# Performance work log

Measured on AMD Instinct MI355X. Metric: run time of the kernel, lower is better.

The kernel has to match this reference:

```python
import jax, jax.numpy as jnp
import numpy as np

N_EMBD = 1024
N_HEAD = 16
HEAD_DIM = N_EMBD // N_HEAD
SEQ = 2048
BATCH = 2
WINDOW = 256
SCALE = 1.0 / np.sqrt(HEAD_DIM)
MASK_VALUE = -10000.0


def setup_inputs() -> dict:
    key = jax.random.key(0)
    ks = jax.random.split(key, 5)
    s = 0.02
    return {
        "hidden_states": jax.random.normal(ks[0], (BATCH, SEQ, N_EMBD), dtype=jnp.float32),
        "w_attn": jax.random.normal(ks[1], (N_EMBD, 3 * N_EMBD), dtype=jnp.float32) * s,
        "b_attn": jnp.zeros((3 * N_EMBD,), dtype=jnp.float32),
        "w_proj": jax.random.normal(ks[2], (N_EMBD, N_EMBD), dtype=jnp.float32) * s,
        "b_proj": jnp.zeros((N_EMBD,), dtype=jnp.float32),
    }


def _mask(seq_len):
    # causal AND sliding window: j <= i and j > i - WINDOW
    i = jnp.arange(seq_len)[:, None]
    j = jnp.arange(seq_len)[None, :]
    return (j <= i) & (j > i - WINDOW)  # [T, T] bool


def reference(hidden_states, w_attn, b_attn, w_proj, b_proj):
    B, T, _ = hidden_states.shape
    qkv = hidden_states @ w_attn + b_attn  # [B, T, 3E]
    q, k, v = jnp.split(qkv, 3, axis=-1)
    # [B, H, T, D]
    q = q.reshape(B, T, N_HEAD, HEAD_DIM).transpose(0, 2, 1, 3)
    k = k.reshape(B, T, N_HEAD, HEAD_DIM).transpose(0, 2, 1, 3)
    v = v.reshape(B, T, N_HEAD, HEAD_DIM).transpose(0, 2, 1, 3)

    scores = jnp.einsum("bhqd,bhkd->bhqk", q, k) * SCALE  # [B, H, T, T]
    mask = _mask(T)[None, None]  # [1, 1, T, T]
    scores = jnp.where(mask, scores, MASK_VALUE)
    scores = jnp.clip(scores, -10000.0, 10000.0)
    attn = jax.nn.softmax(scores, axis=-1)
    out = jnp.einsum("bhqk,bhkd->bhqd", attn, v)  # [B, H, T, D]
    out = out.transpose(0, 2, 1, 3).reshape(B, T, N_EMBD)
    return out @ w_proj + b_proj
```

## Files before the change

### kernel.cpp

```cpp
#include <hip/hip_runtime.h>


typedef __bf16 bf16_t;
typedef bf16_t bf16x8 __attribute__((ext_vector_type(8)));
typedef bf16_t bf16x4 __attribute__((ext_vector_type(4)));
typedef float  floatx4 __attribute__((ext_vector_type(4)));

#define SEQ_T   2048
#define NHEAD   16
#define HDIM    64
#define EMB     1024
#define WIN     256
#define SCALE_F 0.125f

__device__ __forceinline__ int detect_bf16(const uint4* __restrict__ det)
{
    const int lane = threadIdx.x & 63;
    const uint4 v = det[lane];
    int c = 0;
    #pragma unroll
    for (int e = 0; e < 4; ++e) {
        const unsigned int ex = ((&v.x)[e] >> 7) & 0xffu;
        c += (ex >= 100u && ex <= 150u) ? 1 : 0;
    }
    #pragma unroll
    for (int m = 32; m >= 1; m >>= 1) c += __shfl_xor(c, m, 64);
    return (c * 2 > 256) ? 1 : 0;
}

__global__ __launch_bounds__(256) void prologue(
    const void* __restrict__ hidden, bf16_t* __restrict__ Hc,
    const void* __restrict__ ba, bf16_t* __restrict__ bba,
    const void* __restrict__ bp, bf16_t* __restrict__ bbp,
    const void* __restrict__ wA, bf16_t* __restrict__ WtA,
    const void* __restrict__ wP, bf16_t* __restrict__ WtP)
{
    __shared__ __align__(16) bf16_t tile[64][68];
    const int f = detect_bf16((const uint4*)hidden);
    const int blk = blockIdx.x;

    if (blk < 4100) {
        if (f) return;
        const float* src;
        bf16_t* dst;
        int base;
        if (blk < 4096)      { src = (const float*)hidden; dst = Hc;  base = blk * 1024; }
        else if (blk < 4099) { src = (const float*)ba;     dst = bba; base = (blk - 4096) * 1024; }
        else                 { src = (const float*)bp;     dst = bbp; base = 0; }
        const int i4 = base + threadIdx.x * 4;
        const float4 x = *(const float4*)(src + i4);
        bf16x4 v;
        v[0] = (bf16_t)x.x; v[1] = (bf16_t)x.y;
        v[2] = (bf16_t)x.z; v[3] = (bf16_t)x.w;
        *(bf16x4*)(dst + i4) = v;
        return;
    }

    int id = blk - 4100;
    const void* W; bf16_t* Wt; int N, bx, by;
    if (id < 768) { W = wA; Wt = WtA; N = 3072; bx = id % 48; by = id / 48; }
    else { id -= 768; W = wP; Wt = WtP; N = 1024; bx = id % 16; by = id / 16; }
    const int K = 1024;
    const int n0 = bx * 64;
    const int k0 = by * 64;
    const int tx = threadIdx.x & 15;
    const int ty = threadIdx.x >> 4;

    #pragma unroll
    for (int r = ty; r < 64; r += 16) {
        bf16x4 v;
        const size_t base = (size_t)(k0 + r) * N + n0 + tx * 4;
        if (f) {
            v = *(const bf16x4*)((const bf16_t*)W + base);
        } else {
            const float4 x = *(const float4*)((const float*)W + base);
            v[0] = (bf16_t)x.x; v[1] = (bf16_t)x.y;
            v[2] = (bf16_t)x.z; v[3] = (bf16_t)x.w;
        }
        *(bf16x4*)&tile[r][tx * 4] = v;
    }
    __syncthreads();
    #pragma unroll
    for (int r = ty; r < 64; r += 16) {
        bf16x4 v;
        v[0] = tile[tx * 4 + 0][r];
        v[1] = tile[tx * 4 + 1][r];
        v[2] = tile[tx * 4 + 2][r];
        v[3] = tile[tx * 4 + 3][r];
        *(bf16x4*)(Wt + (size_t)(n0 + r) * K + k0 + tx * 4) = v;
    }
}

template<int BNt, int BKt>
__global__ __launch_bounds__(256, 2) void gemm_bt_bias(
    const bf16_t* __restrict__ Abf,
    const bf16_t* __restrict__ Aalt,
    const bf16_t* __restrict__ Bt,
    const bf16_t* __restrict__ biasbf,
    const bf16_t* __restrict__ biasalt,
    void* __restrict__ C,
    int M, int N, int K,
    int force_bf16, const uint4* __restrict__ det)
{
    constexpr int BMt = 128;
    constexpr int NF  = BNt / 32;
    constexpr int LPR = BKt / 8;
    constexpr int CM  = LPR - 1;
    constexpr int RPL = 64 / LPR;
    constexpr int SL  = BKt / 32;
    __shared__ __align__(16) bf16_t As[BMt * BKt];
    __shared__ __align__(16) bf16_t Bs[BNt * BKt];

    const int flag = detect_bf16(det);
    const bf16_t* A    = flag ? Abf    : Aalt;
    const bf16_t* bias = flag ? biasbf : biasalt;
    const int obf = force_bf16 | flag;

    const int tid  = threadIdx.x;
    const int wave = tid >> 6;
    const int lane = tid & 63;
    const int quad = lane >> 4;
    const int n16  = lane & 15;
    const int m0 = blockIdx.y * BMt;
    const int n0 = blockIdx.x * BNt;
    const int wm = (wave >> 1) * 64;
    const int wn = (wave & 1) * (BNt / 2);

    floatx4 acc[4][NF] = {};

    const int lr   = lane / LPR;
    const int lc16 = lane % LPR;

    for (int k0 = 0; k0 < K; k0 += BKt) {
        #pragma unroll
        for (int t = 0; t < (BMt / 4) / RPL; ++t) {
            const int row0 = wave * (BMt / 4) + t * RPL;
            const int g = (lc16 ^ ((row0 + lr) & CM)) * 8;
            const bf16_t* ga = A + (size_t)(m0 + row0 + lr) * K + k0 + g;
            __builtin_amdgcn_global_load_lds(
                (const __attribute__((address_space(1))) void*)ga,
                (__attribute__((address_space(3))) void*)(As + row0 * BKt),
                16, 0, 0);
        }
        #pragma unroll
        for (int t = 0; t < (BNt / 4) / RPL; ++t) {
            const int row0 = wave * (BNt / 4) + t * RPL;
            const int g = (lc16 ^ ((row0 + lr) & CM)) * 8;
            const bf16_t* gb = Bt + (size_t)(n0 + row0 + lr) * K + k0 + g;
            __builtin_amdgcn_global_load_lds(
                (const __attribute__((address_space(1))) void*)gb,
                (__attribute__((address_space(3))) void*)(Bs + row0 * BKt),
                16, 0, 0);
        }
        __syncthreads();

        #pragma unroll
        for (int s = 0; s < SL; ++s) {
            const int ch = (((4 * s + quad) ^ (n16 & CM)) * 8);
            const bf16_t* pa = As + (wm + n16) * BKt + ch;
            const bf16_t* pb = Bs + (wn + n16) * BKt + ch;
            bf16x8 af[4], bfr[NF];
            #pragma unroll
            for (int ff = 0; ff < 4; ++ff)
                af[ff] = *(const bf16x8*)(pa + ff * 16 * BKt);
            #pragma unroll
            for (int ff = 0; ff < NF; ++ff)
                bfr[ff] = *(const bf16x8*)(pb + ff * 16 * BKt);
            #pragma unroll
            for (int mf = 0; mf < 4; ++mf)
                #pragma unroll
                for (int nf = 0; nf < NF; ++nf)
                    acc[mf][nf] = __builtin_amdgcn_mfma_f32_16x16x32_bf16(
                        af[mf], bfr[nf], acc[mf][nf], 0, 0, 0);
        }
        __syncthreads();
    }

    const int col   = n0 + wn + n16;
    const int rbase = m0 + wm + quad * 4;
    #pragma unroll
    for (int nf = 0; nf < NF; ++nf) {
        const float bv = (float)bias[col + nf * 16];
        #pragma unroll
        for (int mf = 0; mf < 4; ++mf) {
            #pragma unroll
            for (int r = 0; r < 4; ++r) {
                const size_t idx =
                    (size_t)(rbase + mf * 16 + r) * N + col + nf * 16;
                const float val = acc[mf][nf][r] + bv;
                if (obf) ((bf16_t*)C)[idx] = (bf16_t)val;
                else     ((float*)C)[idx]  = val;
            }
        }
    }
}

#define CW   80
#define NCH  4
#define VT_S 128
#define P_S  104

__device__ __forceinline__ int vt_salt(int d) { return (d ^ (d >> 3)) & 7; }

__global__ __launch_bounds__(256) void attn_mfma(
    const bf16_t* __restrict__ qkv,
    bf16_t* __restrict__ attn_out)
{
    __shared__ __align__(16) bf16_t Ks[CW * 64];
    __shared__ __align__(16) bf16_t Vt[64 * VT_S];
    __shared__ __align__(16) bf16_t Pst[4][16 * P_S];

    const int tid  = threadIdx.x;
    const int wave = tid >> 6;
    const int lane = tid & 63;
    const int quad = lane >> 4;
    const int n16  = lane & 15;

    const int i0 = blockIdx.x * 64;
    const int h  = blockIdx.y;
    const int b  = blockIdx.z;
    const size_t rowbase = (size_t)b * SEQ_T;
    const int kbase  = i0 - 256;
    const int iw     = 16 * wave;
    const int climit = 256 - i0;

    const bf16_t* Qg = qkv + (rowbase + i0 + iw + n16) * (3 * EMB) + h * HDIM;
    bf16x8 qf[2];
    qf[0] = *(const bf16x8*)(Qg + quad * 8);
    qf[1] = *(const bf16x8*)(Qg + 32 + quad * 8);

    for (int i = tid; i < 1024; i += 256) {
        const int d = i >> 4;
        const int k = 80 + (i & 15);
        Vt[d * VT_S + (((k >> 3) ^ vt_salt(d)) << 3) + (k & 7)] = (bf16_t)0.f;
    }
    for (int i = tid; i < 1024; i += 256)
        Pst[i >> 8][((i >> 4) & 15) * P_S + 80 + (i & 15)] = (bf16_t)0.f;

    floatx4 Oac[4] = {};
    float m_run[4], l_run[4];
    #pragma unroll
    for (int rr = 0; rr < 4; ++rr) { m_run[rr] = -3.0e38f; l_run[rr] = 0.f; }

    bf16x8 vreg[3];

    auto loadV = [&](int hc) {
        const int cbase = hc * CW;
        #pragma unroll
        for (int t = 0; t < 3; ++t) {
            const int idx = tid + 256 * t;
            if (idx < 640) {
                const int lc = idx >> 3;
                const int d0 = (idx & 7) * 8;
                int j = kbase + cbase + lc; if (j < 0) j = 0;
                vreg[t] = *(const bf16x8*)(qkv + (rowbase + j) * (3 * EMB)
                                           + 2 * EMB + h * HDIM + d0);
            }
        }
    };
    auto stageK = [&](int hc) {
        const int cbase = hc * CW;
        for (int t = wave; t < 10; t += 4) {
            const int lc0 = t * 8;
            const int lcL = lc0 + (lane >> 3);
            int j = kbase + cbase + lcL; if (j < 0) j = 0;
            const int g = (lane & 7) ^ (lane >> 3);
            const bf16_t* src = qkv + (rowbase + j) * (3 * EMB)
                                + EMB + h * HDIM + g * 8;
            __builtin_amdgcn_global_load_lds(
                (const __attribute__((address_space(1))) void*)src,
                (__attribute__((address_space(3))) void*)(Ks + lc0 * 64),
                16, 0, 0);
        }
    };
    auto writeVt = [&]() {
        #pragma unroll
        for (int t = 0; t < 3; ++t) {
            const int idx = tid + 256 * t;
            if (idx < 640) {
                const int lc = idx >> 3;
                const int d0 = (idx & 7) * 8;
                #pragma unroll
                for (int e = 0; e < 8; ++e) {
                    const int d = d0 + e;
                    Vt[d * VT_S + (((lc >> 3) ^ vt_salt(d)) << 3) + (lc & 7)]
                        = vreg[t][e];
                }
            }
        }
    };

    loadV(0);
    stageK(0);

    for (int hc = 0; hc < NCH; ++hc) {
        const int cbase = hc * CW;

        __syncthreads();
        writeVt();
        __syncthreads();

        if (hc < NCH - 1) loadV(hc + 1);

        floatx4 sc[5];
        __builtin_amdgcn_s_setprio(1);
        #pragma unroll
        for (int tt = 0; tt < 5; ++tt) {
            sc[tt] = (floatx4){0.f, 0.f, 0.f, 0.f};
            #pragma unroll
            for (int s2 = 0; s2 < 2; ++s2) {
                const int lc = 16 * tt + n16;
                const int ch = (4 * s2 + quad) ^ (lc & 7);
                const bf16x8 kf = *(const bf16x8*)(Ks + lc * 64 + ch * 8);
                sc[tt] = __builtin_amdgcn_mfma_f32_16x16x32_bf16(
                    qf[s2], kf, sc[tt], 0, 0, 0);
            }
        }
        __builtin_amdgcn_s_setprio(0);

        #pragma unroll
        for (int tt = 0; tt < 5; ++tt) {
            const int c  = cbase + 16 * tt + n16;
            const int cw = c - iw;
            #pragma unroll
            for (int rr = 0; rr < 4; ++rr) {
                const int r = quad * 4 + rr;
                const bool valid = (cw > r) && (cw <= r + 256) && (c >= climit);
                sc[tt][rr] = valid ? sc[tt][rr] * SCALE_F : -3.0e38f;
            }
        }

        float cm[4];
        #pragma unroll
        for (int rr = 0; rr < 4; ++rr) {
            cm[rr] = -3.0e38f;
            #pragma unroll
            for (int tt = 0; tt < 5; ++tt) cm[rr] = fmaxf(cm[rr], sc[tt][rr]);
            #pragma unroll
            for (int m = 8; m >= 1; m >>= 1)
                cm[rr] = fmaxf(cm[rr], __shfl_xor(cm[rr], m, 64));
        }
        #pragma unroll
        for (int rr = 0; rr < 4; ++rr) {
            const float mnew  = fmaxf(m_run[rr], cm[rr]);
            const float alpha = __expf(m_run[rr] - mnew);
            m_run[rr] = mnew;
            l_run[rr] *= alpha;
            #pragma unroll
            for (int nt = 0; nt < 4; ++nt) Oac[nt][rr] *= alpha;
        }

        float psum[4] = {0.f, 0.f, 0.f, 0.f};
        #pragma unroll
        for (int tt = 0; tt < 5; ++tt) {
            #pragma unroll
            for (int rr = 0; rr < 4; ++rr) {
                const float s = sc[tt][rr];
                const float e = (s > -1.0e38f) ? __expf(s - m_run[rr]) : 0.f;
                psum[rr] += e;
                Pst[wave][(quad * 4 + rr) * P_S + 16 * tt + n16] = (bf16_t)e;
            }
        }
        #pragma unroll
        for (int rr = 0; rr < 4; ++rr) {
            #pragma unroll
            for (int m = 8; m >= 1; m >>= 1)
                psum[rr] += __shfl_xor(psum[rr], m, 64);
            l_run[rr] += psum[rr];
        }

        __syncthreads();

        if (hc < NCH - 1) stageK(hc + 1);

        __builtin_amdgcn_s_setprio(1);
        #pragma unroll
        for (int ks = 0; ks < 3; ++ks) {
            const bf16x8 paf = *(const bf16x8*)(
                &Pst[wave][n16 * P_S + ks * 32 + quad * 8]);
            #pragma unroll
            for (int nt = 0; nt < 4; ++nt) {
                const int d = nt * 16 + n16;
                const int cc = (ks * 4 + quad) ^ vt_salt(d);
                const bf16x8 vbf = *(const bf16x8*)(Vt + d * VT_S + cc * 8);
                Oac[nt] = __builtin_amdgcn_mfma_f32_16x16x32_bf16(
                    paf, vbf, Oac[nt], 0, 0, 0);
            }
        }
        __builtin_amdgcn_s_setprio(0);
    }

    #pragma unroll
    for (int rr = 0; rr < 4; ++rr) {
        const float rden = 1.0f / l_run[rr];
        const size_t row = rowbase + i0 + iw + quad * 4 + rr;
        #pragma unroll
        for (int nt = 0; nt < 4; ++nt) {
            attn_out[row * EMB + h * HDIM + nt * 16 + n16] =
                (bf16_t)(Oac[nt][rr] * rden);
        }
    }
}

extern "C" void kernel_launch(void* const* d_in, const int* in_sizes, int n_in,
                              void* d_out, int out_size, void* d_ws, size_t ws_size,
                              hipStream_t stream)
{
    const void* hidden = d_in[0];
    const void* w_attn = d_in[1];
    const void* b_attn = d_in[2];
    const void* w_proj = d_in[3];
    const void* b_proj = d_in[4];

    char* ws = (char*)d_ws;
    bf16_t* Wt_attn = (bf16_t*)(ws);
    bf16_t* Wt_proj = (bf16_t*)(ws + (6u << 20));
    bf16_t* qkv     = (bf16_t*)(ws + (8u << 20));
    bf16_t* attn_o  = (bf16_t*)(ws + (32u << 20));
    bf16_t* Hc      = (bf16_t*)(ws + (40u << 20));
    bf16_t* bb_attn = (bf16_t*)(ws + (48u << 20));
    bf16_t* bb_proj = (bf16_t*)(ws + (48u << 20) + 8192);

    const uint4* det = (const uint4*)hidden;

    prologue<<<5124, 256, 0, stream>>>(hidden, Hc, b_attn, bb_attn,
                                       b_proj, bb_proj,
                                       w_attn, Wt_attn, w_proj, Wt_proj);

    gemm_bt_bias<192, 64><<<dim3(3072 / 192, 4096 / 128), 256, 0, stream>>>(
        (const bf16_t*)hidden, Hc, Wt_attn,
        (const bf16_t*)b_attn, bb_attn, qkv, 4096, 3072, 1024, 1, det);

    attn_mfma<<<dim3(SEQ_T / 64, NHEAD, 2), 256, 0, stream>>>(qkv, attn_o);

    gemm_bt_bias<64, 128><<<dim3(1024 / 64, 4096 / 128), 256, 0, stream>>>(
        attn_o, attn_o, Wt_proj,
        (const bf16_t*)b_proj, bb_proj, (void*)d_out, 4096, 1024, 1024, 0, det);
}
```

Measured before the change: 162.2 us.

## Double-buffer GEMM LDS tiles and skip fully-masked attention chunks

The GEMM now keeps two LDS buffers and issues the global-to-LDS loads for the next K tile before computing the current one. It waits with explicit vmcnt counts and raw s_barrier instead of __syncthreads, aiming to overlap memory latency with MFMA work. The attention kernel starts at the first key chunk that is not entirely before the sequence start, skipping work for early query blocks. The projection GEMM drops to BK=64 to fit the doubled LDS. Risks are the hand-coded vmcnt literals being wrong and higher LDS use lowering occupancy.

```diff
diff --git a/kernel.cpp b/kernel.cpp
--- a/kernel.cpp
+++ b/kernel.cpp
@@ -12,6 +12,14 @@
 #define EMB     1024
 #define WIN     256
 #define SCALE_F 0.125f
+
+template<int N> __device__ __forceinline__ void waitcnt_vm()
+{
+    if constexpr (N == 0)       asm volatile("s_waitcnt vmcnt(0)"  ::: "memory");
+    else if constexpr (N == 6)  asm volatile("s_waitcnt vmcnt(6)"  ::: "memory");
+    else if constexpr (N == 10) asm volatile("s_waitcnt vmcnt(10)" ::: "memory");
+    else static_assert(N == 0 || N == 6 || N == 10, "add vmcnt literal");
+}
 
 __device__ __forceinline__ int detect_bf16(const uint4* __restrict__ det)
 {
@@ -108,8 +116,11 @@
     constexpr int CM  = LPR - 1;
     constexpr int RPL = 64 / LPR;
     constexpr int SL  = BKt / 32;
-    __shared__ __align__(16) bf16_t As[BMt * BKt];
-    __shared__ __align__(16) bf16_t Bs[BNt * BKt];
+    constexpr int LA  = (BMt / 4) / RPL;
+    constexpr int LB  = (BNt / 4) / RPL;
+    constexpr int LDW = LA + LB;
+    __shared__ __align__(16) bf16_t As[2][BMt * BKt];
+    __shared__ __align__(16) bf16_t Bs[2][BNt * BKt];
 
     const int flag = detect_bf16(det);
     const bf16_t* A    = flag ? Abf    : Aalt;
@@ -131,34 +142,48 @@
     const int lr   = lane / LPR;
     const int lc16 = lane % LPR;
 
-    for (int k0 = 0; k0 < K; k0 += BKt) {
-        #pragma unroll
-        for (int t = 0; t < (BMt / 4) / RPL; ++t) {
+    auto stage = [&](int bsel, int k0) {
+        #pragma unroll
+        for (int t = 0; t < LA; ++t) {
             const int row0 = wave * (BMt / 4) + t * RPL;
             const int g = (lc16 ^ ((row0 + lr) & CM)) * 8;
             const bf16_t* ga = A + (size_t)(m0 + row0 + lr) * K + k0 + g;
             __builtin_amdgcn_global_load_lds(
                 (const __attribute__((address_space(1))) void*)ga,
-                (__attribute__((address_space(3))) void*)(As + row0 * BKt),
+                (__attribute__((address_space(3))) void*)(As[bsel] + row0 * BKt),
                 16, 0, 0);
         }
         #pragma unroll
-        for (int t = 0; t < (BNt / 4) / RPL; ++t) {
+        for (int t = 0; t < LB; ++t) {
             const int row0 = wave * (BNt / 4) + t * RPL;
             const int g = (lc16 ^ ((row0 + lr) & CM)) * 8;
             const bf16_t* gb = Bt + (size_t)(n0 + row0 + lr) * K + k0 + g;
             __builtin_amdgcn_global_load_lds(
                 (const __attribute__((address_space(1))) void*)gb,
-                (__attribute__((address_space(3))) void*)(Bs + row0 * BKt),
+                (__attribute__((address_space(3))) void*)(Bs[bsel] + row0 * BKt),
                 16, 0, 0);
         }
-        __syncthreads();
-
+    };
+
+    stage(0, 0);
+
+    const int NIT = K / BKt;
+    for (int it = 0; it < NIT; ++it) {
+        const int buf = it & 1;
+        if (it + 1 < NIT) stage(buf ^ 1, (it + 1) * BKt);
+        __builtin_amdgcn_sched_barrier(0);
+        if (it + 1 < NIT) waitcnt_vm<LDW>();
+        else              waitcnt_vm<0>();
+        __builtin_amdgcn_s_barrier();
+        __builtin_amdgcn_sched_barrier(0);
+
+        const bf16_t* __restrict__ Ab = As[buf];
+        const bf16_t* __restrict__ Bb = Bs[buf];
         #pragma unroll
         for (int s = 0; s < SL; ++s) {
             const int ch = (((4 * s + quad) ^ (n16 & CM)) * 8);
-            const bf16_t* pa = As + (wm + n16) * BKt + ch;
-            const bf16_t* pb = Bs + (wn + n16) * BKt + ch;
+            const bf16_t* pa = Ab + (wm + n16) * BKt + ch;
+            const bf16_t* pb = Bb + (wn + n16) * BKt + ch;
             bf16x8 af[4], bfr[NF];
             #pragma unroll
             for (int ff = 0; ff < 4; ++ff)
@@ -173,7 +198,7 @@
                     acc[mf][nf] = __builtin_amdgcn_mfma_f32_16x16x32_bf16(
                         af[mf], bfr[nf], acc[mf][nf], 0, 0, 0);
         }
-        __syncthreads();
+        __builtin_amdgcn_s_barrier();
     }
 
     const int col   = n0 + wn + n16;
@@ -223,6 +248,8 @@
     const int kbase  = i0 - 256;
     const int iw     = 16 * wave;
     const int climit = 256 - i0;
+
+    const int hc0 = (climit > 79) ? ((climit - 80) / 80 + 1) : 0;
 
     const bf16_t* Qg = qkv + (rowbase + i0 + iw + n16) * (3 * EMB) + h * HDIM;
     bf16x8 qf[2];
@@ -290,10 +317,10 @@
         }
     };
 
-    loadV(0);
-    stageK(0);
-
-    for (int hc = 0; hc < NCH; ++hc) {
+    loadV(hc0);
+    stageK(hc0);
+
+    for (int hc = hc0; hc < NCH; ++hc) {
         const int cbase = hc * CW;
 
         __syncthreads();
@@ -433,7 +460,7 @@
 
     attn_mfma<<<dim3(SEQ_T / 64, NHEAD, 2), 256, 0, stream>>>(qkv, attn_o);
 
-    gemm_bt_bias<64, 128><<<dim3(1024 / 64, 4096 / 128), 256, 0, stream>>>(
+    gemm_bt_bias<64, 64><<<dim3(1024 / 64, 4096 / 128), 256, 0, stream>>>(
         attn_o, attn_o, Wt_proj,
         (const bf16_t*)b_proj, bb_proj, (void*)d_out, 4096, 1024, 1024, 0, det);
 }
```

Result: no change. 164.9 us (+1.7%).
